# Optimization experiments

Hardware: AMD Instinct MI355X
Metric: run time of the kernel (lower is better)

Reference implementation:

```python
import jax, jax.numpy as jnp
import numpy as np

N = 20000      # nodes
E = 400000     # edges
D = 256        # input_dim == hidden_dim
L = 4          # num_layers
EIN = 32       # edgenet_input_dim // 2
EH = 128       # edge parser hidden
NC = 2         # num_classes
JK = L * D     # 1024
BN_EPS = 1e-5


def setup_inputs() -> dict:
    key = jax.random.key(0)
    ks = jax.random.split(key, 16)
    s = 0.05
    inp = {
        "features": jax.random.normal(ks[0], (N, D), jnp.float32),
        "edge_index": jax.random.randint(ks[1], (2, E), 0, N, dtype=jnp.int64),
        "edgenet_input": jax.random.normal(ks[2], (E, 2 * EIN), jnp.float32),
        # ChebConv weights: [layer, k, in, out] (all layers 256->256, K=3, no bias)
        "cheb_w": jax.random.normal(ks[3], (L, 3, D, D), jnp.float32) * s,
        # EdgeEncoder (PAE-style) parser: Linear(32,128)+ReLU+BN+Linear(128,128)
        "en_w1": jax.random.normal(ks[4], (EIN, EH), jnp.float32) * s,
        "en_b1": jnp.zeros((EH,), jnp.float32),
        "en_g1": jnp.ones((EH,), jnp.float32),
        "en_be1": jnp.zeros((EH,), jnp.float32),
        "en_w2": jax.random.normal(ks[5], (EH, EH), jnp.float32) * s,
        "en_b2": jnp.zeros((EH,), jnp.float32),
        # cls head: Linear(1024,256)+ReLU+BN(256)+Linear(256,2)
        "cls_w1": jax.random.normal(ks[6], (JK, 256), jnp.float32) * s,
        "cls_b1": jnp.zeros((256,), jnp.float32),
        "cls_g": jnp.ones((256,), jnp.float32),
        "cls_b": jnp.zeros((256,), jnp.float32),
        "cls_w2": jax.random.normal(ks[7], (256, NC), jnp.float32) * s,
        "cls_b2": jnp.zeros((NC,), jnp.float32),
    }
    return inp


def _bn_eval(x, g, b):
    # eval-mode BatchNorm1d with fresh running stats (mean=0, var=1)
    return x * (g / jnp.sqrt(1.0 + BN_EPS)) + b


def reference(features, edge_index, edgenet_input, cheb_w,
              en_w1, en_b1, en_g1, en_be1, en_w2, en_b2,
              cls_w1, cls_b1, cls_g, cls_b, cls_w2, cls_b2):
    row, col = edge_index[0], edge_index[1]

    # ---- EdgeEncoder (PAE): shared parser on both halves + cosine sim ----
    def parser(x):
        h = jnp.maximum(x @ en_w1 + en_b1, 0.0)
        h = _bn_eval(h, en_g1, en_be1)
        return h @ en_w2 + en_b2

    half = edgenet_input.shape[1] // 2
    h1 = parser(edgenet_input[:, :half])
    h2 = parser(edgenet_input[:, half:])
    n1 = jnp.maximum(jnp.linalg.norm(h1, axis=1), 1e-8)
    n2 = jnp.maximum(jnp.linalg.norm(h2, axis=1), 1e-8)
    cos = jnp.sum(h1 * h2, axis=1) / (n1 * n2)
    edge_weight = (cos + 1.0) * 0.5  # [E]

    # ---- ChebConv sym normalization (lambda_max=2): L_hat = -D^-1/2 A D^-1/2 ----
    deg = jax.ops.segment_sum(edge_weight, row, num_segments=N)
    dis = jnp.where(deg > 0, jax.lax.rsqrt(jnp.maximum(deg, 1e-30)), 0.0)
    norm = -dis[row] * edge_weight * dis[col]  # [E]

    def prop(x):  # out[col] += norm * x[row]
        return jax.ops.segment_sum(x[row] * norm[:, None], col, num_segments=N)

    # ---- stacked ChebConv (K=3, no bias) + ReLU + JK concat ----
    x = features
    jk = None
    for i in range(L):
        W = cheb_w[i]
        Tx0 = x
        Tx1 = prop(Tx0)
        Tx2 = 2.0 * prop(Tx1) - Tx0
        h = jnp.maximum(Tx0 @ W[0] + Tx1 @ W[1] + Tx2 @ W[2], 0.0)
        jk = h if i == 0 else jnp.concatenate([jk, h], axis=1)
        x = h

    # ---- cls head ----
    z = jnp.maximum(jk @ cls_w1 + cls_b1, 0.0)
    z = _bn_eval(z, cls_g, cls_b)
    logit = z @ cls_w2 + cls_b2
    return (logit, edge_weight)
```

## Files before the change

### kernel.cpp

```cpp
#include <hip/hip_runtime.h>
#include <hip/hip_bf16.h>

#define NN 20000
#define EE 400000
#define RSBN 0.9999950000374997f

typedef __attribute__((ext_vector_type(8))) short short8;
typedef __attribute__((ext_vector_type(8))) unsigned short ushort8;
typedef __attribute__((ext_vector_type(4))) short bf4;
typedef __attribute__((ext_vector_type(4))) float floatx4;

__device__ __forceinline__ short f2bf(float f) {
  union { float f; unsigned u; } v; v.f = f;
  unsigned r = v.u + 0x7fffu + ((v.u >> 16) & 1u);
  return (short)(r >> 16);
}
__device__ __forceinline__ unsigned f2bf2(float x, float y) {
  union { __hip_bfloat162 h; unsigned u; } v;
  v.h = __float22bfloat162_rn(make_float2(x, y));
  return v.u;
}
__device__ __forceinline__ float bf2f(unsigned short u) {
  union { unsigned u; float f; } v; v.u = ((unsigned)u) << 16;
  return v.f;
}
__device__ __forceinline__ void gl_lds16(const void* g, void* l) {
  __builtin_amdgcn_global_load_lds(
      (const __attribute__((address_space(1))) unsigned*)g,
      (__attribute__((address_space(3))) unsigned*)l, 16, 0, 0);
}

__device__ __forceinline__ floatx4 mfma16(bf4 a, bf4 b, floatx4 c) {
#if __has_builtin(__builtin_amdgcn_mfma_f32_16x16x16bf16_1k)
  return __builtin_amdgcn_mfma_f32_16x16x16bf16_1k(a, b, c, 0, 0, 0);
#else
  floatx4 d;
  asm volatile("v_mfma_f32_16x16x16_bf16 %0, %1, %2, %3"
               : "=&v"(d) : "v"(a), "v"(b), "v"(c));
  return d;
#endif
}

__device__ __forceinline__ float dpp_xor1(float x) {
  union { float f; int i; } a, b;
  a.f = x;
  b.i = __builtin_amdgcn_update_dpp(0, a.i, 0xB1, 0xF, 0xF, false);
  return b.f;
}

__global__ __launch_bounds__(256) void ewconv_kernel(
    const float* __restrict__ w1, const float* __restrict__ w2,
    const float* __restrict__ g1, const float* __restrict__ be1,
    const float* __restrict__ b1, const float* __restrict__ b2,
    unsigned short* __restrict__ ewf)
{
  int tid = threadIdx.x;
#pragma unroll
  for (int i = 0; i < 16; i++) {
    int idx = i * 256 + tid;
    int k = idx >> 7, n = idx & 127;
    int pos = ((n >> 4) * 64 + (k >> 3) * 16 + (n & 15)) * 8 + (k & 7);
    ewf[pos] = f2bf(w1[idx]);
  }
#pragma unroll
  for (int i = 0; i < 64; i++) {
    int idx = i * 256 + tid;
    int k = idx >> 7, n = idx & 127;
    int u = k >> 4, q = (k >> 2) & 3, j = k & 3;
    int t = n >> 4, l = n & 15;
    int pos = (((u * 8 + t) * 4 + q) * 16 + l) * 4 + j;
    ewf[4096 + pos] = f2bf(w2[idx] * g1[k] * RSBN);
  }
  float* fb = (float*)(ewf + 20480);
  if (tid < 128) {
    fb[tid] = b1[tid];
    float acc = b2[tid];
    for (int k = 0; k < 128; k++) acc += be1[k] * w2[k * 128 + tid] * g1[k] * RSBN;
    fb[128 + tid] = acc;
  }
}

__global__ __launch_bounds__(512, 4) void edge_kernel(
    const float* __restrict__ xin, const int* __restrict__ eidx,
    const unsigned short* __restrict__ ewf,
    float* __restrict__ ew_out,
    float* __restrict__ deg, int* __restrict__ cnt)
{
  __shared__ short wbuf[20992];

  int tid = threadIdx.x;
  int lane = tid & 63;
  int wv = tid >> 6;
  int l15 = lane & 15;
  int quad = lane >> 4;

#pragma unroll
  for (int i = 0; i < 5; i++)
    gl_lds16(ewf + (i * 512 + tid) * 8, &wbuf[(i * 512 + tid) * 8]);
  if (tid < 64)
    gl_lds16(ewf + (2560 + tid) * 8, &wbuf[(2560 + tid) * 8]);

  const short* w1f = wbuf;
  const short* w2f = wbuf + 4096;

  int rowA = blockIdx.x * 256 + wv * 16;
  int rowB = rowA + 128;

  short8 afA, afB;
  {
    const float* xpA = xin + (size_t)(rowA + l15) * 32 + quad * 8;
    const float* xpB = xin + (size_t)(rowB + l15) * 32 + quad * 8;
    float4 a0 = *(const float4*)xpA;
    float4 a1 = *(const float4*)(xpA + 4);
    float4 b0 = *(const float4*)xpB;
    float4 b1v = *(const float4*)(xpB + 4);
    union { short8 s; unsigned u[4]; } a, b;
    a.u[0] = f2bf2(a0.x, a0.y); a.u[1] = f2bf2(a0.z, a0.w);
    a.u[2] = f2bf2(a1.x, a1.y); a.u[3] = f2bf2(a1.z, a1.w);
    b.u[0] = f2bf2(b0.x, b0.y); b.u[1] = f2bf2(b0.z, b0.w);
    b.u[2] = f2bf2(b1v.x, b1v.y); b.u[3] = f2bf2(b1v.z, b1v.w);
    afA = a.s; afB = b.s;
  }

  __syncthreads();

  const float* fb = (const float*)(wbuf + 20480);

  floatx4 acc1A[8], acc1B[8];
#pragma unroll
  for (int t = 0; t < 8; t++) {
    floatx4 z = *(const floatx4*)&fb[t * 16 + quad * 4];
    short8 w1v = *(const short8*)&w1f[(t * 64 + lane) * 8];
    acc1A[t] = __builtin_amdgcn_mfma_f32_16x16x32_bf16(w1v, afA, z, 0, 0, 0);
    acc1B[t] = __builtin_amdgcn_mfma_f32_16x16x32_bf16(w1v, afB, z, 0, 0, 0);
  }

  bf4 pbA[8], pbB[8];
#pragma unroll
  for (int u = 0; u < 8; u++) {
    union { bf4 s; unsigned w[2]; } oa, ob;
    oa.w[0] = f2bf2(fmaxf(acc1A[u][0], 0.f), fmaxf(acc1A[u][1], 0.f));
    oa.w[1] = f2bf2(fmaxf(acc1A[u][2], 0.f), fmaxf(acc1A[u][3], 0.f));
    ob.w[0] = f2bf2(fmaxf(acc1B[u][0], 0.f), fmaxf(acc1B[u][1], 0.f));
    ob.w[1] = f2bf2(fmaxf(acc1B[u][2], 0.f), fmaxf(acc1B[u][3], 0.f));
    pbA[u] = oa.s; pbB[u] = ob.s;
  }

  floatx4 acc2A[8], acc2B[8];
#pragma unroll
  for (int t = 0; t < 8; t++) {
    floatx4 z2 = *(const floatx4*)&fb[128 + t * 16 + quad * 4];
    acc2A[t] = z2; acc2B[t] = z2;
  }
#pragma unroll
  for (int u = 0; u < 8; u++)
#pragma unroll
    for (int t = 0; t < 8; t++) {
      bf4 a4 = *(const bf4*)&w2f[((u * 8 + t) * 64 + lane) * 4];
      acc2A[t] = mfma16(a4, pbA[u], acc2A[t]);
      acc2B[t] = mfma16(a4, pbB[u], acc2B[t]);
    }

#pragma unroll
  for (int tile = 0; tile < 2; tile++) {
    floatx4* acc2 = tile ? acc2B : acc2A;
    int rowbase = tile ? rowB : rowA;
    float qq = 0.f, pp = 0.f;
#pragma unroll
    for (int t = 0; t < 8; t++)
#pragma unroll
      for (int r = 0; r < 4; r++) {
        float h = acc2[t][r];
        float hp = dpp_xor1(h);
        qq += h * h;
        pp += h * hp;
      }
    qq += __shfl_xor(qq, 16, 64);
    pp += __shfl_xor(pp, 16, 64);
    qq += __shfl_xor(qq, 32, 64);
    pp += __shfl_xor(pp, 32, 64);
    float rr = dpp_xor1(qq);

    if (quad == 0 && !(l15 & 1)) {
      int e = (rowbase + l15) >> 1;
      float n1 = fmaxf(sqrtf(qq), 1e-8f);
      float n2 = fmaxf(sqrtf(rr), 1e-8f);
      float w = (pp / (n1 * n2) + 1.f) * 0.5f;
      ew_out[e] = w;
      atomicAdd(deg + eidx[e], w);
      atomicAdd(cnt + eidx[EE + e], 1);
    }
  }
}

__global__ __launch_bounds__(256) void fconv_kernel(const float* __restrict__ src,
                                                    unsigned short* __restrict__ dst) {
  size_t i = ((size_t)blockIdx.x * 256 + threadIdx.x) * 8;
  float4 a = *(const float4*)(src + i);
  float4 b = *(const float4*)(src + i + 4);
  union { ushort8 s; unsigned u[4]; } o;
  o.u[0] = f2bf2(a.x, a.y); o.u[1] = f2bf2(a.z, a.w);
  o.u[2] = f2bf2(b.x, b.y); o.u[3] = f2bf2(b.z, b.w);
  *(ushort8*)(dst + i) = o.s;
}

__global__ __launch_bounds__(256) void wconv_kernel(
    const float* __restrict__ cheb_w, const float* __restrict__ cls_w1,
    unsigned short* __restrict__ wtc, unsigned short* __restrict__ clsT)
{
  __shared__ unsigned short tile[64][80];
  int z = blockIdx.z;
  const float* src; unsigned short* dst; int ldk;
  if (z < 12) {
    int l = z / 3, c = z % 3;
    src = cheb_w + (size_t)z * 65536;
    dst = wtc + (size_t)l * 196608 + c * 256;
    ldk = 768;
  } else {
    int c = z - 12;
    src = cls_w1 + (size_t)c * 65536;
    dst = clsT + c * 256;
    ldk = 1024;
  }
  int t = threadIdx.x;
  int k0 = blockIdx.x * 64, n0 = blockIdx.y * 64;
#pragma unroll
  for (int pass = 0; pass < 4; pass++) {
    int kk = pass * 16 + (t >> 4);
    int nl = (t & 15) * 4;
    float4 v = *(const float4*)(src + (size_t)(k0 + kk) * 256 + n0 + nl);
    tile[nl + 0][kk] = f2bf(v.x);
    tile[nl + 1][kk] = f2bf(v.y);
    tile[nl + 2][kk] = f2bf(v.z);
    tile[nl + 3][kk] = f2bf(v.w);
  }
  __syncthreads();
  int nl = t >> 2, kc = (t & 3) * 16;
  ushort8 v0 = *(const ushort8*)&tile[nl][kc];
  ushort8 v1 = *(const ushort8*)&tile[nl][kc + 8];
  unsigned short* dp = dst + (size_t)(n0 + nl) * ldk + k0 + kc;
  *(ushort8*)dp = v0;
  *(ushort8*)(dp + 8) = v1;
}

__global__ __launch_bounds__(1024) void scan_kernel(const int* __restrict__ cnt, int* __restrict__ ptr) {
  __shared__ int sums[1024];
  int tid = threadIdx.x;
  const int n = NN;
  const int chunk = (n + 1023) / 1024;
  int base = tid * chunk;
  int s = 0;
  for (int i = 0; i < chunk; i++) {
    int idx = base + i;
    if (idx < n) s += (cnt[idx] + 3) & ~3;
  }
  sums[tid] = s;
  __syncthreads();
  for (int off = 1; off < 1024; off <<= 1) {
    int v = (tid >= off) ? sums[tid - off] : 0;
    __syncthreads();
    sums[tid] += v;
    __syncthreads();
  }
  int run = (tid == 0) ? 0 : sums[tid - 1];
  for (int i = 0; i < chunk; i++) {
    int idx = base + i;
    if (idx < n) { ptr[idx] = run; run += (cnt[idx] + 3) & ~3; }
  }
  if (tid == 1023) ptr[n] = run;
}

__global__ __launch_bounds__(256) void hist_kernel(const int* __restrict__ cnt,
                                                   int* __restrict__ hist) {
  __shared__ int lh[64];
  int tid = threadIdx.x;
  if (tid < 64) lh[tid] = 0;
  __syncthreads();
  int i = blockIdx.x * 256 + tid;
  if (i < NN) {
    int b = (cnt[i] + 3) >> 2; if (b > 63) b = 63;
    atomicAdd(&lh[b], 1);
  }
  __syncthreads();
  if (tid < 64 && lh[tid]) atomicAdd(&hist[tid], lh[tid]);
}

__global__ void binscan_kernel(const int* __restrict__ hist,
                               int* __restrict__ binbase, int* __restrict__ binfill) {
  int tid = threadIdx.x;
  int v = hist[tid];
  int x = v;
#pragma unroll
  for (int off = 1; off < 64; off <<= 1) {
    int y = __shfl_up(x, off, 64);
    if (tid >= off) x += y;
  }
  binbase[tid] = x - v;
  binfill[tid] = 0;
}

__global__ __launch_bounds__(256) void perm_kernel(const int* __restrict__ cnt,
                                                   const int* __restrict__ binbase,
                                                   int* __restrict__ binfill,
                                                   int* __restrict__ perm) {
  __shared__ int lh[64], lbase[64];
  int tid = threadIdx.x;
  if (tid < 64) lh[tid] = 0;
  __syncthreads();
  int i = blockIdx.x * 256 + tid;
  int b = 0, local = 0;
  bool valid = (i < NN);
  if (valid) {
    b = (cnt[i] + 3) >> 2; if (b > 63) b = 63;
    local = atomicAdd(&lh[b], 1);
  }
  __syncthreads();
  if (tid < 64 && lh[tid]) lbase[tid] = atomicAdd(&binfill[tid], lh[tid]);
  __syncthreads();
  if (valid) perm[binbase[b] + lbase[b] + local] = i;
}

__global__ void fill_kernel(const int* __restrict__ eidx, const float* __restrict__ ew,
                            const float* __restrict__ deg, const int* __restrict__ ptr,
                            int* __restrict__ fill, int* __restrict__ cidx, float* __restrict__ cval) {
  int e = blockIdx.x * 256 + threadIdx.x;
  if (e < EE) {
    int r = eidx[e], c = eidx[EE + e];
    float dr = deg[r], dc = deg[c];
    float ir = dr > 0.f ? 1.f / sqrtf(fmaxf(dr, 1e-30f)) : 0.f;
    float ic = dc > 0.f ? 1.f / sqrtf(fmaxf(dc, 1e-30f)) : 0.f;
    float nv = -ir * ew[e] * ic;
    int pos = ptr[c] + atomicAdd(&fill[c], 1);
    cidx[pos] = r;
    cval[pos] = nv;
  }
}

__global__ __launch_bounds__(256) void prop_kernel(
    const unsigned short* __restrict__ x, int ldx,
    const int* __restrict__ cidx, const float* __restrict__ cval,
    const int* __restrict__ ptr, const int* __restrict__ perm,
    unsigned short* __restrict__ y, int ldy,
    float alpha, const unsigned short* __restrict__ sub, int ldsub)
{
  int sliceid = blockIdx.x & 7;
  int colslice = sliceid >> 1;
  int chunk = (blockIdx.x >> 3) * 2 + (sliceid & 1);
  int ci = chunk * 32 + (threadIdx.x >> 3);
  if (ci >= NN) return;
  int c = perm[ci];
  int d = colslice * 64 + (threadIdx.x & 7) * 8;
  int p0 = ptr[c], p1 = ptr[c + 1];
  float a[8] = {0.f, 0.f, 0.f, 0.f, 0.f, 0.f, 0.f, 0.f};

#define PLOAD(P, R, W, V0, V1, V2, V3)                                  \
  do {                                                                  \
    R = *(const int4*)(cidx + (P));                                     \
    W = *(const float4*)(cval + (P));                                   \
    V0 = *(const ushort8*)(x + (size_t)R.x * ldx + d);                  \
    V1 = *(const ushort8*)(x + (size_t)R.y * ldx + d);                  \
    V2 = *(const ushort8*)(x + (size_t)R.z * ldx + d);                  \
    V3 = *(const ushort8*)(x + (size_t)R.w * ldx + d);                  \
  } while (0)

#define PACC(W, V0, V1, V2, V3)                                         \
  do {                                                                  \
    _Pragma("unroll")                                                   \
    for (int j = 0; j < 8; j++)                                         \
      a[j] += W.x * bf2f(V0[j]) + W.y * bf2f(V1[j]) +                   \
              W.z * bf2f(V2[j]) + W.w * bf2f(V3[j]);                    \
  } while (0)

  if (p0 < p1) {
    int n4 = (p1 - p0) >> 2;
    int4 rA, rB; float4 wA, wB;
    ushort8 vA0, vA1, vA2, vA3, vB0, vB1, vB2, vB3;
    PLOAD(p0, rA, wA, vA0, vA1, vA2, vA3);
    if (n4 == 1) {
      PACC(wA, vA0, vA1, vA2, vA3);
    } else {
      PLOAD(p0 + 4, rB, wB, vB0, vB1, vB2, vB3);
      int p = p0 + 8;
      if (n4 & 1) {
        PACC(wA, vA0, vA1, vA2, vA3);
        PLOAD(p, rA, wA, vA0, vA1, vA2, vA3);
        p += 4;
      }
      for (; p < p1; p += 8) {
        PACC(wA, vA0, vA1, vA2, vA3);
        PLOAD(p, rA, wA, vA0, vA1, vA2, vA3);
        PACC(wB, vB0, vB1, vB2, vB3);
        PLOAD(p + 4, rB, wB, vB0, vB1, vB2, vB3);
      }
      PACC(wA, vA0, vA1, vA2, vA3);
      PACC(wB, vB0, vB1, vB2, vB3);
    }
  }
#undef PLOAD
#undef PACC

  union { ushort8 s; unsigned u[4]; } o;
  if (sub) {
    ushort8 sv = *(const ushort8*)(sub + (size_t)c * ldsub + d);
#pragma unroll
    for (int j = 0; j < 8; j += 2)
      o.u[j >> 1] = f2bf2(alpha * a[j] - bf2f(sv[j]), alpha * a[j + 1] - bf2f(sv[j + 1]));
  } else {
#pragma unroll
    for (int j = 0; j < 8; j += 2)
      o.u[j >> 1] = f2bf2(a[j], a[j + 1]);
  }
  *(ushort8*)(y + (size_t)c * ldy + d) = o.s;
}

__global__ __launch_bounds__(256, 4) void mgemm_kernel(
    const unsigned short* A0, const unsigned short* A1,
    const unsigned short* A2, const unsigned short* A3,
    int l0, int l1, int l2, int l3, int nchunks,
    const unsigned short* __restrict__ BT, int ldbt,
    unsigned short* __restrict__ Cb, float* __restrict__ Cf, int ldc, int M,
    const float* __restrict__ bias, const float* __restrict__ bng,
    const float* __restrict__ bnb)
{
  __shared__ short As[4 * 64 * 8];
  __shared__ short Bs[4 * 128 * 8];
  int tid = threadIdx.x;
  int lane = tid & 63;
  int wv = tid >> 6;
  int l15 = lane & 15, quad = lane >> 4;
  int wr = wv >> 1, wc = wv & 1;
  int m0 = blockIdx.x * 64, n0 = blockIdx.y * 128;

  const unsigned short* Ap[4] = {A0, A1, A2, A3};
  int Al[4] = {l0, l1, l2, l3};

  int arow = tid & 63, ac = tid >> 6;
  int brow = tid & 127, bc = tid >> 7;

  floatx4 acc[2][4];
#pragma unroll
  for (int mi = 0; mi < 2; mi++)
#pragma unroll
    for (int nj = 0; nj < 4; nj++) acc[mi][nj] = (floatx4){0.f, 0.f, 0.f, 0.f};

  for (int c = 0; c < nchunks; c++) {
    const unsigned short* Abase = Ap[c] + (size_t)(m0 + arow) * Al[c] + ac * 8;
    const unsigned short* Bbase = BT + (size_t)(n0 + brow) * ldbt + c * 256 + bc * 8;
#pragma unroll 1
    for (int kb = 0; kb < 256; kb += 32) {
      __syncthreads();
      gl_lds16(Abase + kb, &As[tid * 8]);
      gl_lds16(Bbase + kb, &Bs[tid * 8]);
      gl_lds16(Bbase + 16 + kb, &Bs[(tid + 256) * 8]);
      __syncthreads();
      short8 af[2], bfv[4];
#pragma unroll
      for (int mi = 0; mi < 2; mi++)
        af[mi] = *(const short8*)&As[(quad * 64 + wr * 32 + mi * 16 + l15) * 8];
#pragma unroll
      for (int nj = 0; nj < 4; nj++)
        bfv[nj] = *(const short8*)&Bs[(quad * 128 + wc * 64 + nj * 16 + l15) * 8];
#pragma unroll
      for (int nj = 0; nj < 4; nj++)
#pragma unroll
        for (int mi = 0; mi < 2; mi++)
          acc[mi][nj] = __builtin_amdgcn_mfma_f32_16x16x32_bf16(af[mi], bfv[nj], acc[mi][nj], 0, 0, 0);
    }
  }

  if (Cb) {
#pragma unroll
    for (int mi = 0; mi < 2; mi++)
#pragma unroll
      for (int r = 0; r < 4; r++) {
        int row = m0 + wr * 32 + mi * 16 + quad * 4 + r;
        if (row < M) {
#pragma unroll
          for (int nj = 0; nj < 4; nj++) {
            int col = n0 + wc * 64 + nj * 16 + l15;
            Cb[(size_t)row * ldc + col] = (unsigned short)f2bf(fmaxf(acc[mi][nj][r], 0.f));
          }
        }
      }
  } else {
    float bs[4], g[4], bb[4];
#pragma unroll
    for (int nj = 0; nj < 4; nj++) {
      int col = n0 + wc * 64 + nj * 16 + l15;
      bs[nj] = bias[col]; g[nj] = bng[col] * RSBN; bb[nj] = bnb[col];
    }
#pragma unroll
    for (int mi = 0; mi < 2; mi++)
#pragma unroll
      for (int r = 0; r < 4; r++) {
        int row = m0 + wr * 32 + mi * 16 + quad * 4 + r;
        if (row < M) {
#pragma unroll
          for (int nj = 0; nj < 4; nj++) {
            int col = n0 + wc * 64 + nj * 16 + l15;
            float v = fmaxf(acc[mi][nj][r] + bs[nj], 0.f) * g[nj] + bb[nj];
            Cf[(size_t)row * ldc + col] = v;
          }
        }
      }
  }
}

__global__ __launch_bounds__(256) void logit_kernel(
    const float* __restrict__ z, const float* __restrict__ w2,
    const float* __restrict__ b2, float* __restrict__ out)
{
  int node = blockIdx.x * 4 + (threadIdx.x >> 6);
  if (node >= NN) return;
  int lane = threadIdx.x & 63;
  int k = lane * 4;
  float4 zv = *(const float4*)(z + (size_t)node * 256 + k);
  float4 wa = *(const float4*)(w2 + k * 2);
  float4 wb = *(const float4*)(w2 + k * 2 + 4);
  float a0 = zv.x * wa.x + zv.y * wa.z + zv.z * wb.x + zv.w * wb.z;
  float a1 = zv.x * wa.y + zv.y * wa.w + zv.z * wb.y + zv.w * wb.w;
#pragma unroll
  for (int m = 32; m >= 1; m >>= 1) {
    a0 += __shfl_xor(a0, m, 64);
    a1 += __shfl_xor(a1, m, 64);
  }
  if (lane == 0) {
    out[(size_t)node * 2]     = a0 + b2[0];
    out[(size_t)node * 2 + 1] = a1 + b2[1];
  }
}

extern "C" void kernel_launch(void* const* d_in, const int* in_sizes, int n_in,
                              void* d_out, int out_size, void* d_ws, size_t ws_size,
                              hipStream_t stream) {
  const float* features = (const float*)d_in[0];
  const int*   eidx     = (const int*)d_in[1];
  const float* xin      = (const float*)d_in[2];
  const float* cheb_w   = (const float*)d_in[3];
  const float* en_w1    = (const float*)d_in[4];
  const float* en_b1    = (const float*)d_in[5];
  const float* en_g1    = (const float*)d_in[6];
  const float* en_be1   = (const float*)d_in[7];
  const float* en_w2    = (const float*)d_in[8];
  const float* en_b2    = (const float*)d_in[9];
  const float* cls_w1   = (const float*)d_in[10];
  const float* cls_b1   = (const float*)d_in[11];
  const float* cls_g    = (const float*)d_in[12];
  const float* cls_b    = (const float*)d_in[13];
  const float* cls_w2   = (const float*)d_in[14];
  const float* cls_b2   = (const float*)d_in[15];
  float* out = (float*)d_out;

  char* ws = (char*)d_ws;
  size_t off = 0;
  auto alloc = [&](size_t bytes) -> void* {
    void* p = ws + off;
    off += (bytes + 255) & ~(size_t)255;
    return p;
  };
  const int CSRN = EE + 4 * NN;
  float* deg  = (float*)alloc((size_t)NN * 4);
  int*   cnt  = (int*)  alloc((size_t)NN * 4);
  int*   fil  = (int*)  alloc((size_t)NN * 4);
  int*   hist = (int*)  alloc(64 * 4);
  float* cval = (float*)alloc((size_t)CSRN * 4);
  int*   cidx = (int*)  alloc((size_t)CSRN * 4);
  size_t zero_len = off;
  int*   ptr  = (int*)  alloc((size_t)(NN + 1) * 4);
  int*   perm = (int*)  alloc((size_t)NN * 4);
  int*   binbase = (int*)alloc(64 * 4);
  int*   binfill = (int*)alloc(64 * 4);
  unsigned short* featb = (unsigned short*)alloc((size_t)NN * 256 * 2);
  unsigned short* Tx1   = (unsigned short*)alloc((size_t)NN * 256 * 2);
  unsigned short* Tx2   = (unsigned short*)alloc((size_t)NN * 256 * 2);
  unsigned short* jk    = (unsigned short*)alloc((size_t)NN * 1024 * 2);
  float* zbuf = (float*)alloc((size_t)NN * 256 * 4);
  unsigned short* wtc   = (unsigned short*)alloc((size_t)4 * 196608 * 2);
  unsigned short* clsT  = (unsigned short*)alloc((size_t)256 * 1024 * 2);
  unsigned short* ewf   = (unsigned short*)alloc((size_t)20992 * 2);
  alloc(262144);

  float* ew = out + (size_t)NN * 2;

  hipMemsetAsync(deg, 0, zero_len, stream);

  ewconv_kernel<<<1, 256, 0, stream>>>(en_w1, en_w2, en_g1, en_be1, en_b1, en_b2, ewf);
  edge_kernel<<<3125, 512, 0, stream>>>(xin, eidx, ewf, ew, deg, cnt);
  fconv_kernel<<<2500, 256, 0, stream>>>(features, featb);
  wconv_kernel<<<dim3(4, 4, 16), 256, 0, stream>>>(cheb_w, cls_w1, wtc, clsT);
  scan_kernel<<<1, 1024, 0, stream>>>(cnt, ptr);
  hist_kernel<<<(NN + 255) / 256, 256, 0, stream>>>(cnt, hist);
  binscan_kernel<<<1, 64, 0, stream>>>(hist, binbase, binfill);
  perm_kernel<<<(NN + 255) / 256, 256, 0, stream>>>(cnt, binbase, binfill, perm);
  fill_kernel<<<(EE + 255) / 256, 256, 0, stream>>>(eidx, ew, deg, ptr, fil, cidx, cval);

  dim3 ggrid(313, 2);
  for (int i = 0; i < 4; i++) {
    const unsigned short* x = (i == 0) ? featb : (jk + (size_t)(i - 1) * 256);
    int ldx = (i == 0) ? 256 : 1024;
    prop_kernel<<<2504, 256, 0, stream>>>(x, ldx, cidx, cval, ptr, perm, Tx1, 256, 1.f, nullptr, 0);
    prop_kernel<<<2504, 256, 0, stream>>>(Tx1, 256, cidx, cval, ptr, perm, Tx2, 256, 2.f, x, ldx);
    mgemm_kernel<<<ggrid, 256, 0, stream>>>(x, Tx1, Tx2, nullptr, ldx, 256, 256, 0, 3,
                                            wtc + (size_t)i * 196608, 768,
                                            jk + (size_t)i * 256, nullptr, 1024, NN,
                                            nullptr, nullptr, nullptr);
  }

  mgemm_kernel<<<ggrid, 256, 0, stream>>>(jk, jk + 256, jk + 512, jk + 768,
                                          1024, 1024, 1024, 1024, 4, clsT, 1024,
                                          nullptr, zbuf, 256, NN,
                                          cls_b1, cls_g, cls_b);
  logit_kernel<<<NN / 4, 256, 0, stream>>>(zbuf, cls_w2, cls_b2, out);
}
```

Measured before the change: 648.2 us.

## Fold Chebyshev recurrence into weights, use 16-bit CSR indices, swizzle GEMM blocks

The Tx2 = 2*prop(Tx1) - Tx0 recurrence is folded into the GEMM weights (W0 - W2 and 2*W2), so the second propagation stores the raw product and no longer reads and subtracts Tx0. CSR column indices are stored as 16-bit values, halving index traffic in the sparse propagation kernels; this relies on the node count fitting in 16 bits. The GEMM block index is also remapped across XCDs to improve L2 locality. Folding the weights changes bf16 rounding of the combined weights slightly.

Result: no change. 638.4 us (-1.5%).

```diff
diff --git a/kernel.cpp b/kernel.cpp
--- a/kernel.cpp
+++ b/kernel.cpp
@@ -46,6 +46,12 @@
   a.f = x;
   b.i = __builtin_amdgcn_update_dpp(0, a.i, 0xB1, 0xF, 0xF, false);
   return b.f;
+}
+
+__device__ __forceinline__ int xcd_swizzle(int bid, int nwg) {
+  int q = nwg >> 3, r = nwg & 7;
+  int x = bid & 7, o = bid >> 3;
+  return (x < r ? x * (q + 1) : r * (q + 1) + (x - r) * q) + o;
 }
 
 __global__ __launch_bounds__(256) void ewconv_kernel(
@@ -210,10 +216,13 @@
 {
   __shared__ unsigned short tile[64][80];
   int z = blockIdx.z;
-  const float* src; unsigned short* dst; int ldk;
+  const float* src; const float* src2 = nullptr; float scale = 1.f;
+  unsigned short* dst; int ldk;
   if (z < 12) {
     int l = z / 3, c = z % 3;
     src = cheb_w + (size_t)z * 65536;
+    if (c == 0) src2 = cheb_w + (size_t)(l * 3 + 2) * 65536;
+    if (c == 2) scale = 2.f;
     dst = wtc + (size_t)l * 196608 + c * 256;
     ldk = 768;
   } else {
@@ -228,7 +237,14 @@
   for (int pass = 0; pass < 4; pass++) {
     int kk = pass * 16 + (t >> 4);
     int nl = (t & 15) * 4;
-    float4 v = *(const float4*)(src + (size_t)(k0 + kk) * 256 + n0 + nl);
+    size_t offe = (size_t)(k0 + kk) * 256 + n0 + nl;
+    float4 v = *(const float4*)(src + offe);
+    if (src2) {
+      float4 v2 = *(const float4*)(src2 + offe);
+      v.x -= v2.x; v.y -= v2.y; v.z -= v2.z; v.w -= v2.w;
+    } else if (scale != 1.f) {
+      v.x *= scale; v.y *= scale; v.z *= scale; v.w *= scale;
+    }
     tile[nl + 0][kk] = f2bf(v.x);
     tile[nl + 1][kk] = f2bf(v.y);
     tile[nl + 2][kk] = f2bf(v.z);
@@ -322,7 +338,8 @@
 
 __global__ void fill_kernel(const int* __restrict__ eidx, const float* __restrict__ ew,
                             const float* __restrict__ deg, const int* __restrict__ ptr,
-                            int* __restrict__ fill, int* __restrict__ cidx, float* __restrict__ cval) {
+                            int* __restrict__ fill, unsigned short* __restrict__ cidx,
+                            float* __restrict__ cval) {
   int e = blockIdx.x * 256 + threadIdx.x;
   if (e < EE) {
     int r = eidx[e], c = eidx[EE + e];
@@ -331,17 +348,16 @@
     float ic = dc > 0.f ? 1.f / sqrtf(fmaxf(dc, 1e-30f)) : 0.f;
     float nv = -ir * ew[e] * ic;
     int pos = ptr[c] + atomicAdd(&fill[c], 1);
-    cidx[pos] = r;
+    cidx[pos] = (unsigned short)r;
     cval[pos] = nv;
   }
 }
 
 __global__ __launch_bounds__(256) void prop_kernel(
     const unsigned short* __restrict__ x, int ldx,
-    const int* __restrict__ cidx, const float* __restrict__ cval,
+    const unsigned short* __restrict__ cidx, const float* __restrict__ cval,
     const int* __restrict__ ptr, const int* __restrict__ perm,
-    unsigned short* __restrict__ y, int ldy,
-    float alpha, const unsigned short* __restrict__ sub, int ldsub)
+    unsigned short* __restrict__ y, int ldy)
 {
   int sliceid = blockIdx.x & 7;
   int colslice = sliceid >> 1;
@@ -355,7 +371,7 @@
 
 #define PLOAD(P, R, W, V0, V1, V2, V3)                                  \
   do {                                                                  \
-    R = *(const int4*)(cidx + (P));                                     \
+    R = *(const ushort4*)(cidx + (P));                                  \
     W = *(const float4*)(cval + (P));                                   \
     V0 = *(const ushort8*)(x + (size_t)R.x * ldx + d);                  \
     V1 = *(const ushort8*)(x + (size_t)R.y * ldx + d);                  \
@@ -373,7 +389,7 @@
 
   if (p0 < p1) {
     int n4 = (p1 - p0) >> 2;
-    int4 rA, rB; float4 wA, wB;
+    ushort4 rA, rB; float4 wA, wB;
     ushort8 vA0, vA1, vA2, vA3, vB0, vB1, vB2, vB3;
     PLOAD(p0, rA, wA, vA0, vA1, vA2, vA3);
     if (n4 == 1) {
@@ -400,16 +416,9 @@
 #undef PACC
 
   union { ushort8 s; unsigned u[4]; } o;
-  if (sub) {
-    ushort8 sv = *(const ushort8*)(sub + (size_t)c * ldsub + d);
-#pragma unroll
-    for (int j = 0; j < 8; j += 2)
-      o.u[j >> 1] = f2bf2(alpha * a[j] - bf2f(sv[j]), alpha * a[j + 1] - bf2f(sv[j + 1]));
-  } else {
-#pragma unroll
-    for (int j = 0; j < 8; j += 2)
-      o.u[j >> 1] = f2bf2(a[j], a[j + 1]);
-  }
+#pragma unroll
+  for (int j = 0; j < 8; j += 2)
+    o.u[j >> 1] = f2bf2(a[j], a[j + 1]);
   *(ushort8*)(y + (size_t)c * ldy + d) = o.s;
 }
 
@@ -429,7 +438,8 @@
   int wv = tid >> 6;
   int l15 = lane & 15, quad = lane >> 4;
   int wr = wv >> 1, wc = wv & 1;
-  int m0 = blockIdx.x * 64, n0 = blockIdx.y * 128;
+  int bidx = xcd_swizzle(blockIdx.x, gridDim.x);
+  int m0 = bidx * 64, n0 = blockIdx.y * 128;
 
   const unsigned short* Ap[4] = {A0, A1, A2, A3};
   int Al[4] = {l0, l1, l2, l3};
@@ -564,7 +574,7 @@
   int*   fil  = (int*)  alloc((size_t)NN * 4);
   int*   hist = (int*)  alloc(64 * 4);
   float* cval = (float*)alloc((size_t)CSRN * 4);
-  int*   cidx = (int*)  alloc((size_t)CSRN * 4);
+  unsigned short* cidx = (unsigned short*)alloc((size_t)CSRN * 2);
   size_t zero_len = off;
   int*   ptr  = (int*)  alloc((size_t)(NN + 1) * 4);
   int*   perm = (int*)  alloc((size_t)NN * 4);
@@ -598,8 +608,8 @@
   for (int i = 0; i < 4; i++) {
     const unsigned short* x = (i == 0) ? featb : (jk + (size_t)(i - 1) * 256);
     int ldx = (i == 0) ? 256 : 1024;
-    prop_kernel<<<2504, 256, 0, stream>>>(x, ldx, cidx, cval, ptr, perm, Tx1, 256, 1.f, nullptr, 0);
-    prop_kernel<<<2504, 256, 0, stream>>>(Tx1, 256, cidx, cval, ptr, perm, Tx2, 256, 2.f, x, ldx);
+    prop_kernel<<<2504, 256, 0, stream>>>(x, ldx, cidx, cval, ptr, perm, Tx1, 256);
+    prop_kernel<<<2504, 256, 0, stream>>>(Tx1, 256, cidx, cval, ptr, perm, Tx2, 256);
     mgemm_kernel<<<ggrid, 256, 0, stream>>>(x, Tx1, Tx2, nullptr, ldx, 256, 256, 0, 3,
                                             wtc + (size_t)i * 196608, 768,
                                             jk + (size_t)i * 256, nullptr, 1024, NN,
```
